# Kernel tuning notes

Measured on AMD Instinct MI355X. Metric: run time of the kernel, lower is better.

## Reference

```python
import jax, jax.numpy as jnp
import numpy as np

DIM = 384
HEADS = 12
HEAD_DIM = DIM // HEADS
WS = 7


def setup_inputs() -> dict:
    key = jax.random.key(0)
    k0, k1, k2, k3, k4 = jax.random.split(key, 5)
    x = jax.random.normal(k0, (16, DIM, 56, 56), dtype=jnp.float32)
    s = 1.0 / np.sqrt(DIM)
    Wqkv = jax.random.normal(k1, (DIM, 3 * DIM), dtype=jnp.float32) * s
    bqkv = jax.random.normal(k2, (3 * DIM,), dtype=jnp.float32) * 0.01
    Wproj = jax.random.normal(k3, (DIM, DIM), dtype=jnp.float32) * s
    bproj = jax.random.normal(k4, (DIM,), dtype=jnp.float32) * 0.01
    return {"x": x, "Wqkv": Wqkv, "bqkv": bqkv, "Wproj": Wproj, "bproj": bproj}


def _window_attention(x, Wqkv, bqkv, Wproj, bproj):
    B, D, H, W = x.shape
    x = jnp.transpose(x, (0, 2, 3, 1))  # (B, H, W, D)
    pad_h = (WS - H % WS) % WS
    pad_w = (WS - W % WS) % WS
    if pad_h or pad_w:
        x = jnp.pad(x, ((0, 0), (0, pad_h), (0, pad_w), (0, 0)))
    Hp, Wp = x.shape[1], x.shape[2]
    nH, nW = Hp // WS, Wp // WS
    # window partition: (B*nH*nW, WS*WS, D)
    xw = x.reshape(B, nH, WS, nW, WS, D).transpose(0, 1, 3, 2, 4, 5)
    windows = xw.reshape(B * nH * nW, WS * WS, D)
    BnW, N, _ = windows.shape
    qkv = windows @ Wqkv + bqkv  # (BnW, N, 3D)
    qkv = qkv.reshape(BnW, N, 3, HEADS, HEAD_DIM).transpose(2, 0, 3, 1, 4)
    q, k, v = qkv[0], qkv[1], qkv[2]  # (BnW, heads, N, hd)
    scale = HEAD_DIM ** -0.5
    attn = jnp.einsum('bhnd,bhmd->bhnm', q, k) * scale
    attn = jax.nn.softmax(attn, axis=-1)
    out = jnp.einsum('bhnm,bhmd->bhnd', attn, v)  # (BnW, heads, N, hd)
    out = out.transpose(0, 2, 1, 3).reshape(BnW, N, D)
    out = out @ Wproj + bproj
    # window reverse
    x = out.reshape(B, nH, nW, WS, WS, D).transpose(0, 1, 3, 2, 4, 5)
    x = x.reshape(B, Hp, Wp, D)
    if pad_h or pad_w:
        x = x[:, :H, :W, :]
    return jnp.transpose(x, (0, 3, 1, 2))  # (B, D, H, W)


def reference(x, Wqkv, bqkv, Wproj, bproj):
    return _window_attention(x, Wqkv, bqkv, Wproj, bproj)
```

## Files before the change

### kernel.cpp

```cpp
#include <hip/hip_runtime.h>

#define TOK     50176
#define NQKV    1152
#define NQKVP   1280
#define DMODEL  384
#define PROJP   512
#define HW      3136
#define NWIN    1024

typedef __bf16 bf16x8 __attribute__((ext_vector_type(8)));
typedef float  f32x4  __attribute__((ext_vector_type(4)));

__device__ __forceinline__ __bf16 f2bf(float f) {
  unsigned u = __float_as_uint(f);
  u += 0x7fffu + ((u >> 16) & 1u);
  unsigned short s = (unsigned short)(u >> 16);
  return __builtin_bit_cast(__bf16, s);
}
__device__ __forceinline__ unsigned short f2bfu(float f) {
  return __builtin_bit_cast(unsigned short, f2bf(f));
}
__device__ __forceinline__ float bf2f(__bf16 b) {
  return __uint_as_float(((unsigned)__builtin_bit_cast(unsigned short, b)) << 16);
}
__device__ __forceinline__ void gload_lds16(const void* g, void* l) {
  __builtin_amdgcn_global_load_lds(
      (const __attribute__((address_space(1))) unsigned int*)g,
      (__attribute__((address_space(3))) unsigned int*)l, 16, 0, 0);
}

__global__ __launch_bounds__(256) void gather_x(const float* __restrict__ x,
                                                __bf16* __restrict__ Xw) {
  __shared__ __bf16 lt[392 * 48];
  const int ct = blockIdx.x, hr = blockIdx.y, b = blockIdx.z;
  const int tid = threadIdx.x;
  const float* xb = x + ((size_t)(b * 384 + ct * 48)) * HW + hr * 7 * 56;

  for (int u = tid; u < 48 * 7 * 14; u += 256) {
    const int ch = u / 98, rem = u % 98;
    const int h7 = rem / 14, w4 = rem % 14;
    const float4 v = *(const float4*)&xb[(size_t)ch * HW + h7 * 56 + 4 * w4];
    const float vv[4] = {v.x, v.y, v.z, v.w};
#pragma unroll
    for (int e = 0; e < 4; ++e) {
      const int w = 4 * w4 + e;
      const int t = (w / 7) * 49 + h7 * 7 + (w % 7);
      lt[t * 48 + ch] = f2bf(vv[e]);
    }
  }
  __syncthreads();

  const size_t tokbase = (size_t)(b * 64 + hr * 8) * 49;
  for (int u = tid; u < 392 * 6; u += 256) {
    const int t = u / 6, c6 = u % 6;
    const bf16x8 vv = *(const bf16x8*)&lt[t * 48 + 8 * c6];
    *(bf16x8*)&Xw[(tokbase + t) * DMODEL + ct * 48 + 8 * c6] = vv;
  }
}

__global__ __launch_bounds__(256) void unscatter(const __bf16* __restrict__ P,
                                                 float* __restrict__ out) {
  __shared__ __bf16 lt[392 * 48];
  const int ct = blockIdx.x, hr = blockIdx.y, b = blockIdx.z;
  const int tid = threadIdx.x;
  const size_t tokbase = (size_t)(b * 64 + hr * 8) * 49;

  for (int u = tid; u < 392 * 6; u += 256) {
    const int t = u / 6, c6 = u % 6;
    *(bf16x8*)&lt[t * 48 + 8 * c6] =
        *(const bf16x8*)&P[(tokbase + t) * PROJP + ct * 48 + 8 * c6];
  }
  __syncthreads();

  float* ob = out + ((size_t)(b * 384 + ct * 48)) * HW + hr * 7 * 56;
  for (int u = tid; u < 48 * 98; u += 256) {
    const int ch = u / 98, rem = u % 98;
    const int h7 = rem / 14, w4 = rem % 14;
    float4 o;
    float* oo = (float*)&o;
#pragma unroll
    for (int e = 0; e < 4; ++e) {
      const int w = 4 * w4 + e;
      const int t = (w / 7) * 49 + h7 * 7 + (w % 7);
      oo[e] = bf2f(lt[t * 48 + ch]);
    }
    *(float4*)&ob[(size_t)ch * HW + h7 * 56 + 4 * w4] = o;
  }
}

__global__ void conv_w(const float* __restrict__ Wqkv, const float* __restrict__ Wproj,
                       const float* __restrict__ bqkv, const float* __restrict__ bproj,
                       __bf16* __restrict__ WqkvT, __bf16* __restrict__ WprojT,
                       float* __restrict__ bqkvP, float* __restrict__ bprojP) {
  const int idx = blockIdx.x * 256 + threadIdx.x;
  if (idx < NQKVP * DMODEL) {
    const int n = idx / DMODEL, k = idx % DMODEL;
    WqkvT[idx] = (n < NQKV) ? f2bf(Wqkv[(size_t)k * NQKV + n]) : (__bf16)0.0f;
  }
  if (idx < PROJP * DMODEL) {
    const int n = idx / DMODEL, k = idx % DMODEL;
    WprojT[idx] = (n < DMODEL) ? f2bf(Wproj[(size_t)k * DMODEL + n]) : (__bf16)0.0f;
  }
  if (idx < NQKVP) bqkvP[idx] = (idx < NQKV) ? bqkv[idx] : 0.f;
  if (idx < PROJP) bprojP[idx] = (idx < DMODEL) ? bproj[idx] : 0.f;
}

__global__ __launch_bounds__(512) void gemm256(const __bf16* __restrict__ A,
                                               const __bf16* __restrict__ BT,
                                               const float* __restrict__ bias,
                                               __bf16* __restrict__ Cout, int Ncols) {
  __shared__ __align__(16) __bf16 As[3][256 * 32];
  __shared__ __align__(16) __bf16 Bs[3][256 * 32];
  const int tid  = threadIdx.x;
  const int lane = tid & 63;
  const int wid  = tid >> 6;

  const int nwg  = gridDim.x * gridDim.y;
  const int orig = blockIdx.y * gridDim.x + blockIdx.x;
  const int q    = nwg >> 3, r = nwg & 7;
  const int xcd  = orig & 7, pos = orig >> 3;
  const int start = (xcd < r) ? xcd * (q + 1) : r * (q + 1) + (xcd - r) * q;
  const int w    = start + pos;
  const int bn   = (w % gridDim.x) << 8;
  const int bm   = (w / gridDim.x) << 8;

  const __bf16* a0 = A  + (size_t)(bm + (tid >> 2)) * DMODEL + ((tid & 3) << 3);
  const __bf16* a1 = a0 + (size_t)128 * DMODEL;
  const __bf16* b0 = BT + (size_t)(bn + (tid >> 2)) * DMODEL + ((tid & 3) << 3);
  const __bf16* b1 = b0 + (size_t)128 * DMODEL;

  const int wm = (wid >> 2) << 7;
  const int wn = (wid & 3) << 6;
  const int lrow = lane & 15;
  const int lk8  = (lane >> 4) << 3;

  f32x4 acc[4][8] = {};

  auto stage = [&](int buf, int kt) {
    const int koff = kt << 5;
    gload_lds16(a0 + koff, &As[buf][(wid << 9)]);
    gload_lds16(a1 + koff, &As[buf][4096 + (wid << 9)]);
    gload_lds16(b0 + koff, &Bs[buf][(wid << 9)]);
    gload_lds16(b1 + koff, &Bs[buf][4096 + (wid << 9)]);
  };

  stage(0, 0);
  stage(1, 1);
  asm volatile("s_waitcnt vmcnt(4)" ::: "memory");
  __builtin_amdgcn_sched_barrier(0);
  __builtin_amdgcn_s_barrier();
  __builtin_amdgcn_sched_barrier(0);

#pragma unroll 1
  for (int kt = 0; kt < 12; ++kt) {
    const int buf = kt % 3;
    const int dst = (kt + 2) % 3;
    const int nt  = (kt + 2 < 12) ? (kt + 2) : (kt - 10);
    stage(dst, nt);

    const __bf16* pA = &As[buf][(wm + lrow) * 32 + lk8];
    const __bf16* pB = &Bs[buf][(wn + lrow) * 32 + lk8];
    bf16x8 av[8], bv[4];
#pragma unroll
    for (int i = 0; i < 8; ++i) av[i] = *(const bf16x8*)(pA + i * 16 * 32);
#pragma unroll
    for (int j = 0; j < 4; ++j) bv[j] = *(const bf16x8*)(pB + j * 16 * 32);
    __builtin_amdgcn_s_setprio(1);
#pragma unroll
    for (int i = 0; i < 8; ++i)
#pragma unroll
      for (int j = 0; j < 4; ++j)
        acc[j][i] = __builtin_amdgcn_mfma_f32_16x16x32_bf16(bv[j], av[i], acc[j][i], 0, 0, 0);
    __builtin_amdgcn_s_setprio(0);
    __builtin_amdgcn_sched_barrier(0);
    asm volatile("s_waitcnt vmcnt(4)" ::: "memory");
    __builtin_amdgcn_sched_barrier(0);
    __builtin_amdgcn_s_barrier();
    __builtin_amdgcn_sched_barrier(0);
  }

  const int lr = lane & 15, g = lane >> 4;
  const int tok0 = bm + wm + lr;
  const int ch0  = bn + wn + (g << 2);

#pragma unroll
  for (int j = 0; j < 4; ++j) {
    const int ch = ch0 + 16 * j;
    const float4 b4 = *(const float4*)&bias[ch];
#pragma unroll
    for (int i = 0; i < 8; ++i) {
      const int token = tok0 + 16 * i;
      ushort4 pk;
      pk.x = f2bfu(acc[j][i][0] + b4.x);
      pk.y = f2bfu(acc[j][i][1] + b4.y);
      pk.z = f2bfu(acc[j][i][2] + b4.z);
      pk.w = f2bfu(acc[j][i][3] + b4.w);
      *(ushort4*)&Cout[(size_t)token * Ncols + ch] = pk;
    }
  }
}

__global__ __launch_bounds__(64) void attn_mfma(const __bf16* __restrict__ qkv,
                                                __bf16* __restrict__ attnO) {
  __shared__ __align__(16) __bf16 lds[96 * 72];
  __bf16* p_lds = lds;
  __bf16* vt    = lds + 64 * 72;

  const int lane = threadIdx.x;
  const int win  = blockIdx.x;
  const int h    = blockIdx.y;
  const int lr = lane & 15, g = lane >> 4;
  const size_t rowbase = (size_t)win * 49;

  int rr[4];
#pragma unroll
  for (int f = 0; f < 4; ++f) rr[f] = (16 * f + lr > 48) ? 48 : (16 * f + lr);

  const int co = h * 32 + 8 * g;

  bf16x8 av[4], bv[4];
#pragma unroll
  for (int f = 0; f < 4; ++f) {
    const __bf16* rp = qkv + (rowbase + rr[f]) * NQKVP + co;
    av[f] = *(const bf16x8*)(rp + 384);
    bv[f] = *(const bf16x8*)(rp);
  }

  ushort4 vreg[7];
#pragma unroll
  for (int u = 0; u < 7; ++u) {
    const int unit = lane + (u << 6);
    if (unit < 392) {
      const int k = unit >> 3, dq = unit & 7;
      vreg[u] = *(const ushort4*)(qkv + (rowbase + k) * NQKVP + 768 + h * 32 + 4 * dq);
    }
  }

  f32x4 acc[4][4] = {};
#pragma unroll
  for (int i = 0; i < 4; ++i)
#pragma unroll
    for (int j = 0; j < 4; ++j)
      acc[i][j] = __builtin_amdgcn_mfma_f32_16x16x32_bf16(av[i], bv[j], acc[i][j], 0, 0, 0);

  const float scale = 0.17677669529663687f;
#pragma unroll
  for (int i = 0; i < 4; ++i)
#pragma unroll
    for (int j = 0; j < 4; ++j)
#pragma unroll
      for (int r = 0; r < 4; ++r) {
        float v = acc[i][j][r] * scale;
        if (i == 3 && (4 * g + r) != 0) v = -1e30f;
        acc[i][j][r] = v;
      }

#pragma unroll
  for (int u = 0; u < 7; ++u) {
    const int unit = lane + (u << 6);
    if (unit < 392) {
      const int k = unit >> 3, dq = unit & 7;
      const ushort4 vv = vreg[u];
      vt[(4 * dq + 0) * 72 + k] = __builtin_bit_cast(__bf16, vv.x);
      vt[(4 * dq + 1) * 72 + k] = __builtin_bit_cast(__bf16, vv.y);
      vt[(4 * dq + 2) * 72 + k] = __builtin_bit_cast(__bf16, vv.z);
      vt[(4 * dq + 3) * 72 + k] = __builtin_bit_cast(__bf16, vv.w);
    }
  }

#pragma unroll
  for (int j = 0; j < 4; ++j) {
    float mx = -1e30f;
#pragma unroll
    for (int i = 0; i < 4; ++i)
#pragma unroll
      for (int r = 0; r < 4; ++r) mx = fmaxf(mx, acc[i][j][r]);
    mx = fmaxf(mx, __shfl_xor(mx, 16));
    mx = fmaxf(mx, __shfl_xor(mx, 32));
    float sum = 0.f;
#pragma unroll
    for (int i = 0; i < 4; ++i)
#pragma unroll
      for (int r = 0; r < 4; ++r) {
        const float e = __expf(acc[i][j][r] - mx);
        acc[i][j][r] = e;
        sum += e;
      }
    sum += __shfl_xor(sum, 16);
    sum += __shfl_xor(sum, 32);
    const float inv = 1.f / sum;
#pragma unroll
    for (int i = 0; i < 4; ++i) {
      ushort4 pk;
      pk.x = f2bfu(acc[i][j][0] * inv);
      pk.y = f2bfu(acc[i][j][1] * inv);
      pk.z = f2bfu(acc[i][j][2] * inv);
      pk.w = f2bfu(acc[i][j][3] * inv);
      *(ushort4*)&p_lds[(16 * j + lr) * 72 + 16 * i + 4 * g] = pk;
    }
  }

  f32x4 o[2][4] = {};
#pragma unroll
  for (int ks = 0; ks < 2; ++ks) {
    bf16x8 a2[2], b2[4];
#pragma unroll
    for (int i2 = 0; i2 < 2; ++i2)
      a2[i2] = *(const bf16x8*)&vt[(16 * i2 + lr) * 72 + 32 * ks + 8 * g];
#pragma unroll
    for (int j2 = 0; j2 < 4; ++j2)
      b2[j2] = *(const bf16x8*)&p_lds[(16 * j2 + lr) * 72 + 32 * ks + 8 * g];
#pragma unroll
    for (int i2 = 0; i2 < 2; ++i2)
#pragma unroll
      for (int j2 = 0; j2 < 4; ++j2)
        o[i2][j2] = __builtin_amdgcn_mfma_f32_16x16x32_bf16(a2[i2], b2[j2], o[i2][j2], 0, 0, 0);
  }

#pragma unroll
  for (int j2 = 0; j2 < 4; ++j2) {
    const int q = 16 * j2 + lr;
    if (q <= 48) {
#pragma unroll
      for (int i2 = 0; i2 < 2; ++i2) {
        ushort4 ok;
        ok.x = f2bfu(o[i2][j2][0]);
        ok.y = f2bfu(o[i2][j2][1]);
        ok.z = f2bfu(o[i2][j2][2]);
        ok.w = f2bfu(o[i2][j2][3]);
        *(ushort4*)&attnO[(rowbase + q) * DMODEL + h * 32 + 16 * i2 + 4 * g] = ok;
      }
    }
  }
}

extern "C" void kernel_launch(void* const* d_in, const int* in_sizes, int n_in,
                              void* d_out, int out_size, void* d_ws, size_t ws_size,
                              hipStream_t stream) {
  const float* x     = (const float*)d_in[0];
  const float* Wqkv  = (const float*)d_in[1];
  const float* bqkv  = (const float*)d_in[2];
  const float* Wproj = (const float*)d_in[3];
  const float* bproj = (const float*)d_in[4];
  float* out = (float*)d_out;

  char* ws = (char*)d_ws;
  __bf16* Xw     = (__bf16*)ws;  ws += (size_t)TOK * DMODEL * 2;
  __bf16* qkvb   = (__bf16*)ws;  ws += (size_t)TOK * NQKVP * 2;
  __bf16* attnO  = (__bf16*)ws;  ws += (size_t)TOK * DMODEL * 2;
  __bf16* attnP  = (__bf16*)ws;  ws += (size_t)TOK * PROJP * 2;
  __bf16* WqkvT  = (__bf16*)ws;  ws += (size_t)NQKVP * DMODEL * 2;
  __bf16* WprojT = (__bf16*)ws;  ws += (size_t)PROJP * DMODEL * 2;
  float*  bqkvP  = (float*)ws;   ws += NQKVP * 4;
  float*  bprojP = (float*)ws;

  gather_x<<<dim3(8, 8, 16), 256, 0, stream>>>(x, Xw);
  conv_w<<<(NQKVP * DMODEL + 255) / 256, 256, 0, stream>>>(Wqkv, Wproj, bqkv, bproj,
                                                           WqkvT, WprojT, bqkvP, bprojP);
  gemm256<<<dim3(NQKVP / 256, TOK / 256), 512, 0, stream>>>(Xw, WqkvT, bqkvP, qkvb, NQKVP);
  attn_mfma<<<dim3(NWIN, 12), 64, 0, stream>>>(qkvb, attnO);
  gemm256<<<dim3(PROJP / 256, TOK / 256), 512, 0, stream>>>(attnO, WprojT, bprojP, attnP, PROJP);
  unscatter<<<dim3(8, 8, 16), 256, 0, stream>>>(attnP, out);
}
```

Baseline: 266.4 us.

## Rewrite GEMM with BK=64 double buffer, swizzled LDS, and 8-phase interleaved schedule

The GEMM now stages K-tiles of 64 into a double-buffered, XOR-swizzled LDS layout instead of triple-buffered K=32 tiles. Each iteration is split into four MFMA quadrants, and the next tile's global-to-LDS loads are interleaved between them so load latency overlaps compute and LDS bank conflicts drop. Output writes are now unpadded (NQKV and DMODEL strides) and masked for padded columns, which shrinks the intermediate buffers read by the attention and unscatter kernels. The extra barriers per iteration add synchronisation overhead.

```diff
diff --git a/kernel.cpp b/kernel.cpp
--- a/kernel.cpp
+++ b/kernel.cpp
@@ -29,6 +29,11 @@
       (__attribute__((address_space(3))) unsigned int*)l, 16, 0, 0);
 }
 
+#define PBAR  do { __builtin_amdgcn_sched_barrier(0); __builtin_amdgcn_s_barrier(); \
+                   __builtin_amdgcn_sched_barrier(0); } while (0)
+#define LGKM0 do { asm volatile("s_waitcnt lgkmcnt(0)" ::: "memory"); \
+                   __builtin_amdgcn_sched_barrier(0); } while (0)
+
 __global__ __launch_bounds__(256) void gather_x(const float* __restrict__ x,
                                                 __bf16* __restrict__ Xw) {
   __shared__ __bf16 lt[392 * 48];
@@ -68,7 +73,7 @@
   for (int u = tid; u < 392 * 6; u += 256) {
     const int t = u / 6, c6 = u % 6;
     *(bf16x8*)&lt[t * 48 + 8 * c6] =
-        *(const bf16x8*)&P[(tokbase + t) * PROJP + ct * 48 + 8 * c6];
+        *(const bf16x8*)&P[(tokbase + t) * DMODEL + ct * 48 + 8 * c6];
   }
   __syncthreads();
 
@@ -105,12 +110,11 @@
   if (idx < PROJP) bprojP[idx] = (idx < DMODEL) ? bproj[idx] : 0.f;
 }
 
-__global__ __launch_bounds__(512) void gemm256(const __bf16* __restrict__ A,
-                                               const __bf16* __restrict__ BT,
-                                               const float* __restrict__ bias,
-                                               __bf16* __restrict__ Cout, int Ncols) {
-  __shared__ __align__(16) __bf16 As[3][256 * 32];
-  __shared__ __align__(16) __bf16 Bs[3][256 * 32];
+__global__ __launch_bounds__(512) void gemm8p(const __bf16* __restrict__ A,
+                                              const __bf16* __restrict__ BT,
+                                              const float* __restrict__ bias,
+                                              __bf16* __restrict__ Cout, int Ncols) {
+  __shared__ __align__(16) __bf16 sm[65536];
   const int tid  = threadIdx.x;
   const int lane = tid & 63;
   const int wid  = tid >> 6;
@@ -124,78 +128,136 @@
   const int bn   = (w % gridDim.x) << 8;
   const int bm   = (w / gridDim.x) << 8;
 
-  const __bf16* a0 = A  + (size_t)(bm + (tid >> 2)) * DMODEL + ((tid & 3) << 3);
-  const __bf16* a1 = a0 + (size_t)128 * DMODEL;
-  const __bf16* b0 = BT + (size_t)(bn + (tid >> 2)) * DMODEL + ((tid & 3) << 3);
-  const __bf16* b1 = b0 + (size_t)128 * DMODEL;
+  const int cswz8 = 8 * ((tid & 7) ^ ((tid >> 3) & 7));
+  const __bf16* aS = A  + (size_t)(bm + (tid >> 3)) * DMODEL + cswz8;
+  const __bf16* bS = BT + (size_t)(bn + (tid >> 3)) * DMODEL + cswz8;
+
+  auto stage_half = [&](int buf, int isB, int h, int kt) {
+    const __bf16* s = (isB ? bS : aS) + (size_t)(h * 128) * DMODEL + (kt << 6);
+    __bf16* d = sm + buf * 32768 + isB * 16384 + h * 8192 + (wid << 9);
+    gload_lds16(s, d);
+    gload_lds16(s + (size_t)64 * DMODEL, d + 4096);
+  };
 
   const int wm = (wid >> 2) << 7;
   const int wn = (wid & 3) << 6;
-  const int lrow = lane & 15;
-  const int lk8  = (lane >> 4) << 3;
+  const int g  = lane >> 4;
+  const int lr = lane & 15;
+  const int sx = lr & 7;
+  const int hA = wm >> 7;
+  const int hB = wn >> 7;
+  const int rB0 = (wn & 64) + lr;
 
   f32x4 acc[4][8] = {};
 
-  auto stage = [&](int buf, int kt) {
-    const int koff = kt << 5;
-    gload_lds16(a0 + koff, &As[buf][(wid << 9)]);
-    gload_lds16(a1 + koff, &As[buf][4096 + (wid << 9)]);
-    gload_lds16(b0 + koff, &Bs[buf][(wid << 9)]);
-    gload_lds16(b1 + koff, &Bs[buf][4096 + (wid << 9)]);
-  };
-
-  stage(0, 0);
-  stage(1, 1);
-  asm volatile("s_waitcnt vmcnt(4)" ::: "memory");
-  __builtin_amdgcn_sched_barrier(0);
-  __builtin_amdgcn_s_barrier();
-  __builtin_amdgcn_sched_barrier(0);
+#pragma unroll
+  for (int t = 0; t < 2; ++t) {
+    stage_half(t, 0, 0, t); stage_half(t, 0, 1, t);
+    stage_half(t, 1, 0, t); stage_half(t, 1, 1, t);
+  }
+  asm volatile("s_waitcnt vmcnt(8)" ::: "memory");
+  PBAR;
 
 #pragma unroll 1
-  for (int kt = 0; kt < 12; ++kt) {
-    const int buf = kt % 3;
-    const int dst = (kt + 2) % 3;
-    const int nt  = (kt + 2 < 12) ? (kt + 2) : (kt - 10);
-    stage(dst, nt);
-
-    const __bf16* pA = &As[buf][(wm + lrow) * 32 + lk8];
-    const __bf16* pB = &Bs[buf][(wn + lrow) * 32 + lk8];
-    bf16x8 av[8], bv[4];
-#pragma unroll
-    for (int i = 0; i < 8; ++i) av[i] = *(const bf16x8*)(pA + i * 16 * 32);
-#pragma unroll
-    for (int j = 0; j < 4; ++j) bv[j] = *(const bf16x8*)(pB + j * 16 * 32);
+  for (int t = 0; t < 6; ++t) {
+    const int buf = t & 1;
+    const int nt  = (t + 2 < 6) ? (t + 2) : (t - 4);
+    const __bf16* Ah = sm + buf * 32768 + hA * 8192;
+    const __bf16* Bh = sm + buf * 32768 + 16384 + hB * 8192;
+
+    bf16x8 av[8][2], bv[4][2];
+
+#pragma unroll
+    for (int i = 0; i < 4; ++i)
+#pragma unroll
+      for (int ks = 0; ks < 2; ++ks)
+        av[i][ks] = *(const bf16x8*)(Ah + (lr + 16 * i) * 64 + 8 * ((4 * ks + g) ^ sx));
+#pragma unroll
+    for (int j = 0; j < 2; ++j)
+#pragma unroll
+      for (int ks = 0; ks < 2; ++ks)
+        bv[j][ks] = *(const bf16x8*)(Bh + (rB0 + 16 * j) * 64 + 8 * ((4 * ks + g) ^ sx));
+    PBAR; LGKM0;
     __builtin_amdgcn_s_setprio(1);
 #pragma unroll
-    for (int i = 0; i < 8; ++i)
-#pragma unroll
-      for (int j = 0; j < 4; ++j)
-        acc[j][i] = __builtin_amdgcn_mfma_f32_16x16x32_bf16(bv[j], av[i], acc[j][i], 0, 0, 0);
+    for (int ks = 0; ks < 2; ++ks)
+#pragma unroll
+      for (int i = 0; i < 4; ++i)
+#pragma unroll
+        for (int j = 0; j < 2; ++j)
+          acc[j][i] = __builtin_amdgcn_mfma_f32_16x16x32_bf16(bv[j][ks], av[i][ks], acc[j][i], 0, 0, 0);
     __builtin_amdgcn_s_setprio(0);
+    PBAR;
+
+#pragma unroll
+    for (int j = 2; j < 4; ++j)
+#pragma unroll
+      for (int ks = 0; ks < 2; ++ks)
+        bv[j][ks] = *(const bf16x8*)(Bh + (rB0 + 16 * j) * 64 + 8 * ((4 * ks + g) ^ sx));
+    PBAR; LGKM0;
+    __builtin_amdgcn_s_setprio(1);
+#pragma unroll
+    for (int ks = 0; ks < 2; ++ks)
+#pragma unroll
+      for (int i = 0; i < 4; ++i)
+#pragma unroll
+        for (int j = 2; j < 4; ++j)
+          acc[j][i] = __builtin_amdgcn_mfma_f32_16x16x32_bf16(bv[j][ks], av[i][ks], acc[j][i], 0, 0, 0);
+    __builtin_amdgcn_s_setprio(0);
+    PBAR;
+
+#pragma unroll
+    for (int i = 4; i < 8; ++i)
+#pragma unroll
+      for (int ks = 0; ks < 2; ++ks)
+        av[i][ks] = *(const bf16x8*)(Ah + (lr + 16 * i) * 64 + 8 * ((4 * ks + g) ^ sx));
+    stage_half(buf, 1, 0, nt);
+    stage_half(buf, 1, 1, nt);
+    PBAR; LGKM0;
+    __builtin_amdgcn_s_setprio(1);
+#pragma unroll
+    for (int ks = 0; ks < 2; ++ks)
+#pragma unroll
+      for (int i = 4; i < 8; ++i)
+#pragma unroll
+        for (int j = 0; j < 2; ++j)
+          acc[j][i] = __builtin_amdgcn_mfma_f32_16x16x32_bf16(bv[j][ks], av[i][ks], acc[j][i], 0, 0, 0);
+    __builtin_amdgcn_s_setprio(0);
+    PBAR;
+
+    stage_half(buf, 0, 0, nt);
+    stage_half(buf, 0, 1, nt);
     __builtin_amdgcn_sched_barrier(0);
-    asm volatile("s_waitcnt vmcnt(4)" ::: "memory");
-    __builtin_amdgcn_sched_barrier(0);
-    __builtin_amdgcn_s_barrier();
-    __builtin_amdgcn_sched_barrier(0);
-  }
-
-  const int lr = lane & 15, g = lane >> 4;
+    asm volatile("s_waitcnt vmcnt(8)" ::: "memory");
+    PBAR;
+    __builtin_amdgcn_s_setprio(1);
+#pragma unroll
+    for (int ks = 0; ks < 2; ++ks)
+#pragma unroll
+      for (int i = 4; i < 8; ++i)
+#pragma unroll
+        for (int j = 2; j < 4; ++j)
+          acc[j][i] = __builtin_amdgcn_mfma_f32_16x16x32_bf16(bv[j][ks], av[i][ks], acc[j][i], 0, 0, 0);
+    __builtin_amdgcn_s_setprio(0);
+    PBAR;
+  }
+
   const int tok0 = bm + wm + lr;
   const int ch0  = bn + wn + (g << 2);
-
 #pragma unroll
   for (int j = 0; j < 4; ++j) {
     const int ch = ch0 + 16 * j;
-    const float4 b4 = *(const float4*)&bias[ch];
-#pragma unroll
-    for (int i = 0; i < 8; ++i) {
-      const int token = tok0 + 16 * i;
-      ushort4 pk;
-      pk.x = f2bfu(acc[j][i][0] + b4.x);
-      pk.y = f2bfu(acc[j][i][1] + b4.y);
-      pk.z = f2bfu(acc[j][i][2] + b4.z);
-      pk.w = f2bfu(acc[j][i][3] + b4.w);
-      *(ushort4*)&Cout[(size_t)token * Ncols + ch] = pk;
+    if (ch < Ncols) {
+      const float4 b4 = *(const float4*)&bias[ch];
+#pragma unroll
+      for (int i = 0; i < 8; ++i) {
+        ushort4 pk;
+        pk.x = f2bfu(acc[j][i][0] + b4.x);
+        pk.y = f2bfu(acc[j][i][1] + b4.y);
+        pk.z = f2bfu(acc[j][i][2] + b4.z);
+        pk.w = f2bfu(acc[j][i][3] + b4.w);
+        *(ushort4*)&Cout[(size_t)(tok0 + 16 * i) * Ncols + ch] = pk;
+      }
     }
   }
 }
@@ -221,7 +283,7 @@
   bf16x8 av[4], bv[4];
 #pragma unroll
   for (int f = 0; f < 4; ++f) {
-    const __bf16* rp = qkv + (rowbase + rr[f]) * NQKVP + co;
+    const __bf16* rp = qkv + (rowbase + rr[f]) * NQKV + co;
     av[f] = *(const bf16x8*)(rp + 384);
     bv[f] = *(const bf16x8*)(rp);
   }
@@ -232,7 +294,7 @@
     const int unit = lane + (u << 6);
     if (unit < 392) {
       const int k = unit >> 3, dq = unit & 7;
-      vreg[u] = *(const ushort4*)(qkv + (rowbase + k) * NQKVP + 768 + h * 32 + 4 * dq);
+      vreg[u] = *(const ushort4*)(qkv + (rowbase + k) * NQKV + 768 + h * 32 + 4 * dq);
     }
   }
 
@@ -346,9 +408,9 @@
 
   char* ws = (char*)d_ws;
   __bf16* Xw     = (__bf16*)ws;  ws += (size_t)TOK * DMODEL * 2;
-  __bf16* qkvb   = (__bf16*)ws;  ws += (size_t)TOK * NQKVP * 2;
+  __bf16* qkvb   = (__bf16*)ws;  ws += (size_t)TOK * NQKV * 2;
   __bf16* attnO  = (__bf16*)ws;  ws += (size_t)TOK * DMODEL * 2;
-  __bf16* attnP  = (__bf16*)ws;  ws += (size_t)TOK * PROJP * 2;
+  __bf16* attnP  = (__bf16*)ws;  ws += (size_t)TOK * DMODEL * 2;
   __bf16* WqkvT  = (__bf16*)ws;  ws += (size_t)NQKVP * DMODEL * 2;
   __bf16* WprojT = (__bf16*)ws;  ws += (size_t)PROJP * DMODEL * 2;
   float*  bqkvP  = (float*)ws;   ws += NQKVP * 4;
@@ -357,8 +419,8 @@
   gather_x<<<dim3(8, 8, 16), 256, 0, stream>>>(x, Xw);
   conv_w<<<(NQKVP * DMODEL + 255) / 256, 256, 0, stream>>>(Wqkv, Wproj, bqkv, bproj,
                                                            WqkvT, WprojT, bqkvP, bprojP);
-  gemm256<<<dim3(NQKVP / 256, TOK / 256), 512, 0, stream>>>(Xw, WqkvT, bqkvP, qkvb, NQKVP);
+  gemm8p<<<dim3(5, TOK / 256), 512, 0, stream>>>(Xw, WqkvT, bqkvP, qkvb, NQKV);
   attn_mfma<<<dim3(NWIN, 12), 64, 0, stream>>>(qkvb, attnO);
-  gemm256<<<dim3(PROJP / 256, TOK / 256), 512, 0, stream>>>(attnO, WprojT, bprojP, attnP, PROJP);
+  gemm8p<<<dim3(2, TOK / 256), 512, 0, stream>>>(attnO, WprojT, bprojP, attnP, DMODEL);
   unscatter<<<dim3(8, 8, 16), 256, 0, stream>>>(attnP, out);
 }
```

New measurement: 249.5 us (median of 4 runs). -6.3%, faster.
